# Optimization experiments

Hardware: AMD Instinct MI355X
Metric: run time of the kernel (lower is better)

## Reference

```python
import jax, jax.numpy as jnp
import numpy as np

N, E, D, R = 50000, 600000, 128, 16
SLOPE = 0.01  # torch default leaky_relu negative slope


def setup_inputs() -> dict:
    key = jax.random.key(0)
    ks = jax.random.split(key, 8)
    return {
        "nfeat": jax.random.normal(ks[0], (N, D), jnp.float32),
        "efeat": jax.random.normal(ks[1], (E, D), jnp.float32),
        # xavier_uniform-ish scale for relation weights / linear layers
        "relation_weight": jax.random.normal(ks[2], (R, D, D), jnp.float32) * (2.0 / np.sqrt(D)),
        "W_res": jax.random.normal(ks[3], (D, D), jnp.float32) / np.sqrt(D),
        "W_res2": jax.random.normal(ks[4], (D, D), jnp.float32) / np.sqrt(D),
        "src": jax.random.randint(ks[5], (E,), 0, N, dtype=jnp.int32),
        "dst": jax.random.randint(ks[6], (E,), 0, N, dtype=jnp.int32),
        "etype": jax.random.randint(ks[7], (E,), 0, R, dtype=jnp.int32),
    }


def reference(nfeat, efeat, relation_weight, W_res, W_res2, src, dst, etype):
    h = nfeat  # feat_drop = 0.0 -> identity
    e = efeat
    # bmm_maybe_select(h[src], W, etype) == (h @ W[r])[src] with r = etype.
    # Precompute all relation projections once: [R, N, D] (avoids E x D x D gather).
    proj = jnp.einsum('nd,rdf->rnf', h, relation_weight)
    t_r = proj[etype, src]   # [E, D]  (tail  * W_r)
    h_r = proj[etype, dst]   # [E, D]  (head  * W_r)
    att = jnp.sum(t_r * jnp.tanh(h_r + e), axis=-1)  # [E] per-edge attention logit
    # edge softmax over incoming edges of each destination node
    seg_max = jax.ops.segment_max(att, dst, num_segments=N)
    ex = jnp.exp(att - seg_max[dst])
    seg_sum = jax.ops.segment_sum(ex, dst, num_segments=N)
    a = ex / seg_sum[dst]                              # [E]
    # message passing: m = h[src] * a, aggregated by sum onto dst
    h_nb = jax.ops.segment_sum(h[src] * a[:, None], dst, num_segments=N)  # [N, D]
    out = (jax.nn.leaky_relu((h + h_nb) @ W_res.T, SLOPE)
           + jax.nn.leaky_relu((h * h_nb) @ W_res2.T, SLOPE))
    return out
```

## Files before the change

kernel.cpp:

```cpp
#include <hip/hip_runtime.h>

#define DF 128

__device__ __forceinline__ float lrelu(float x) { return x > 0.0f ? x : 0.01f * x; }

__global__ __launch_bounds__(256) void k_zero(int* __restrict__ deg,
                                              int* __restrict__ cur, int N) {
  int i = blockIdx.x * 256 + threadIdx.x;
  if (i < N) { deg[i] = 0; cur[i] = 0; }
}

__global__ __launch_bounds__(256) void k_hist(const int* __restrict__ dst,
                                              int* __restrict__ deg, int E) {
  int e = blockIdx.x * 256 + threadIdx.x;
  if (e < E) atomicAdd(&deg[dst[e]], 1);
}

__global__ __launch_bounds__(256) void k_scan1(const int* __restrict__ deg,
                                               int* __restrict__ excl,
                                               int* __restrict__ bsum, int N) {
  __shared__ int s[256];
  int tid = threadIdx.x;
  int i = blockIdx.x * 256 + tid;
  int v = (i < N) ? deg[i] : 0;
  s[tid] = v;
  __syncthreads();
  for (int d = 1; d < 256; d <<= 1) {
    int t = (tid >= d) ? s[tid - d] : 0;
    __syncthreads();
    s[tid] += t;
    __syncthreads();
  }
  int incl = s[tid];
  if (i < N) excl[i] = incl - v;
  if (tid == 255) bsum[blockIdx.x] = incl;
}

__global__ __launch_bounds__(256) void k_scan2(int* __restrict__ bsum, int nb) {
  __shared__ int s[256];
  __shared__ int carry;
  int tid = threadIdx.x;
  if (tid == 0) carry = 0;
  __syncthreads();
  for (int base = 0; base < nb; base += 256) {
    int i = base + tid;
    int v = (i < nb) ? bsum[i] : 0;
    s[tid] = v;
    __syncthreads();
    for (int d = 1; d < 256; d <<= 1) {
      int t = (tid >= d) ? s[tid - d] : 0;
      __syncthreads();
      s[tid] += t;
      __syncthreads();
    }
    int incl = s[tid];
    int c = carry;
    if (i < nb) bsum[i] = incl - v + c;
    __syncthreads();
    if (tid == 255) carry = c + s[255];
    __syncthreads();
  }
}

__global__ __launch_bounds__(256) void k_scan3(const int* __restrict__ excl,
                                               const int* __restrict__ bsum,
                                               int* __restrict__ off, int N, int E) {
  int i = blockIdx.x * 256 + threadIdx.x;
  if (i < N) off[i] = excl[i] + bsum[blockIdx.x];
  if (i == 0) off[N] = E;
}

__global__ __launch_bounds__(256) void k_fill(const int* __restrict__ dst,
                                              const int* __restrict__ off,
                                              int* __restrict__ cur,
                                              int* __restrict__ eid, int E) {
  int e = blockIdx.x * 256 + threadIdx.x;
  if (e >= E) return;
  int d = dst[e];
  int p = atomicAdd(&cur[d], 1);
  eid[off[d] + p] = e;
}

__global__ __launch_bounds__(256) void proj_gemm(const float* __restrict__ h,
                                                 const float* __restrict__ relW,
                                                 float* __restrict__ proj, int N,
                                                 int r0, long long out_rstride) {
  __shared__ float Bs[DF * DF];
  __shared__ float As[32 * DF];
  int r = r0 + blockIdx.y;
  const float* W = relW + (size_t)r * DF * DF;
  float* out = proj + (size_t)blockIdx.y * out_rstride;
  int n0 = blockIdx.x * 32;
  int t = threadIdx.x;

#pragma unroll
  for (int i = 0; i < 16; i++) {
    int idx = i * 256 + t;
    ((float4*)Bs)[idx] = ((const float4*)W)[idx];
  }
#pragma unroll
  for (int i = 0; i < 4; i++) {
    int idx = i * 256 + t;
    int row = idx >> 5, c4 = idx & 31;
    int n = n0 + row;
    float4 v = make_float4(0.f, 0.f, 0.f, 0.f);
    if (n < N) v = ((const float4*)(h + (size_t)n * DF))[c4];
    ((float4*)As)[idx] = v;
  }
  __syncthreads();

  int tc = t & 31, tr = t >> 5;
  float acc[4][4] = {};
#pragma unroll 4
  for (int k = 0; k < DF; k++) {
    float a0 = As[(tr * 4 + 0) * DF + k];
    float a1 = As[(tr * 4 + 1) * DF + k];
    float a2 = As[(tr * 4 + 2) * DF + k];
    float a3 = As[(tr * 4 + 3) * DF + k];
    float4 b = *(const float4*)&Bs[k * DF + tc * 4];
    acc[0][0] += a0 * b.x; acc[0][1] += a0 * b.y; acc[0][2] += a0 * b.z; acc[0][3] += a0 * b.w;
    acc[1][0] += a1 * b.x; acc[1][1] += a1 * b.y; acc[1][2] += a1 * b.z; acc[1][3] += a1 * b.w;
    acc[2][0] += a2 * b.x; acc[2][1] += a2 * b.y; acc[2][2] += a2 * b.z; acc[2][3] += a2 * b.w;
    acc[3][0] += a3 * b.x; acc[3][1] += a3 * b.y; acc[3][2] += a3 * b.z; acc[3][3] += a3 * b.w;
  }
#pragma unroll
  for (int i = 0; i < 4; i++) {
    int n = n0 + tr * 4 + i;
    if (n < N) {
      float4 o = make_float4(acc[i][0], acc[i][1], acc[i][2], acc[i][3]);
      *(float4*)&out[(size_t)n * DF + tc * 4] = o;
    }
  }
}

__global__ __launch_bounds__(256) void att_kernel(const float* __restrict__ proj,
                                                  const float* __restrict__ efeat,
                                                  const int* __restrict__ src,
                                                  const int* __restrict__ dst,
                                                  const int* __restrict__ etype,
                                                  float* __restrict__ att,
                                                  int E, long long rstride, int rsel) {
  int gid = blockIdx.x * 256 + threadIdx.x;
  int e = gid >> 6, lane = gid & 63;
  if (e >= E) return;
  int rt = etype[e];
  if (rsel >= 0 && rt != rsel) return;
  int s = src[e], d = dst[e];
  const float* pb = proj + (size_t)rt * (size_t)rstride;
  float2 tv = ((const float2*)(pb + (size_t)s * DF))[lane];
  float2 hv = ((const float2*)(pb + (size_t)d * DF))[lane];
  float2 ev = ((const float2*)(efeat + (size_t)e * DF))[lane];
  float p = tv.x * tanhf(hv.x + ev.x) + tv.y * tanhf(hv.y + ev.y);
  p += __shfl_down(p, 32);
  p += __shfl_down(p, 16);
  p += __shfl_down(p, 8);
  p += __shfl_down(p, 4);
  p += __shfl_down(p, 2);
  p += __shfl_down(p, 1);
  if (lane == 0) att[e] = p;
}

__global__ __launch_bounds__(256) void gather_kernel(const int* __restrict__ eid,
                                                     const int* __restrict__ off,
                                                     const int* __restrict__ src,
                                                     const float* __restrict__ att,
                                                     const float* __restrict__ nfeat,
                                                     float* __restrict__ h_nb, int N) {
  int node = blockIdx.x * 4 + (threadIdx.x >> 6);
  int lane = threadIdx.x & 63;
  if (node >= N) return;
  int s0 = off[node], s1 = off[node + 1];

  float m = -3.402823466e+38f;
  for (int j = s0 + lane; j < s1; j += 64) {
    float a = att[eid[j]];
    m = fmaxf(m, a);
  }
#pragma unroll
  for (int d = 32; d >= 1; d >>= 1) m = fmaxf(m, __shfl_xor(m, d));

  float2 acc = make_float2(0.f, 0.f);
  float ssum = 0.f;
  for (int j = s0; j < s1; j++) {
    int e = eid[j];
    float ex = expf(att[e] - m);
    int sv = src[e];
    float2 hv = ((const float2*)(nfeat + (size_t)sv * DF))[lane];
    acc.x += hv.x * ex;
    acc.y += hv.y * ex;
    ssum += ex;
  }
  float inv = (s1 > s0) ? 1.0f / ssum : 0.0f;
  float2 o = make_float2(acc.x * inv, acc.y * inv);
  ((float2*)(h_nb + (size_t)node * DF))[lane] = o;
}

__global__ __launch_bounds__(256) void out_gemm(const float* __restrict__ nfeat,
                                                const float* __restrict__ h_nb,
                                                const float* __restrict__ W,
                                                float* __restrict__ out, int N, int mode) {
  __shared__ float Ws[DF * 129];
  __shared__ float As[32 * DF];
  int n0 = blockIdx.x * 32;
  int t = threadIdx.x;
#pragma unroll
  for (int i = 0; i < 16; i++) {
    int idx = i * 256 + t;
    int j = idx >> 5, d4 = idx & 31;
    float4 v = ((const float4*)W)[idx];
    int b = j * 129 + d4 * 4;
    Ws[b + 0] = v.x; Ws[b + 1] = v.y; Ws[b + 2] = v.z; Ws[b + 3] = v.w;
  }
#pragma unroll
  for (int i = 0; i < 4; i++) {
    int idx = i * 256 + t;
    int row = idx >> 5, c4 = idx & 31;
    int n = n0 + row;
    float4 a = make_float4(0.f, 0.f, 0.f, 0.f);
    if (n < N) {
      float4 hv = ((const float4*)(nfeat + (size_t)n * DF))[c4];
      float4 bv = ((const float4*)(h_nb + (size_t)n * DF))[c4];
      if (mode == 0) a = make_float4(hv.x + bv.x, hv.y + bv.y, hv.z + bv.z, hv.w + bv.w);
      else           a = make_float4(hv.x * bv.x, hv.y * bv.y, hv.z * bv.z, hv.w * bv.w);
    }
    ((float4*)As)[idx] = a;
  }
  __syncthreads();

  int tc = t & 31, tr = t >> 5;
  float acc[4][4] = {};
#pragma unroll 4
  for (int k = 0; k < DF; k++) {
    float a0 = As[(tr * 4 + 0) * DF + k];
    float a1 = As[(tr * 4 + 1) * DF + k];
    float a2 = As[(tr * 4 + 2) * DF + k];
    float a3 = As[(tr * 4 + 3) * DF + k];
    float w0 = Ws[(tc * 4 + 0) * 129 + k];
    float w1 = Ws[(tc * 4 + 1) * 129 + k];
    float w2 = Ws[(tc * 4 + 2) * 129 + k];
    float w3 = Ws[(tc * 4 + 3) * 129 + k];
    acc[0][0] += a0 * w0; acc[0][1] += a0 * w1; acc[0][2] += a0 * w2; acc[0][3] += a0 * w3;
    acc[1][0] += a1 * w0; acc[1][1] += a1 * w1; acc[1][2] += a1 * w2; acc[1][3] += a1 * w3;
    acc[2][0] += a2 * w0; acc[2][1] += a2 * w1; acc[2][2] += a2 * w2; acc[2][3] += a2 * w3;
    acc[3][0] += a3 * w0; acc[3][1] += a3 * w1; acc[3][2] += a3 * w2; acc[3][3] += a3 * w3;
  }
#pragma unroll
  for (int i = 0; i < 4; i++) {
    int n = n0 + tr * 4 + i;
    if (n < N) {
      float4 o = make_float4(lrelu(acc[i][0]), lrelu(acc[i][1]),
                             lrelu(acc[i][2]), lrelu(acc[i][3]));
      float4* po = (float4*)&out[(size_t)n * DF + tc * 4];
      if (mode == 0) {
        *po = o;
      } else {
        float4 old = *po;
        *po = make_float4(old.x + o.x, old.y + o.y, old.z + o.z, old.w + o.w);
      }
    }
  }
}

extern "C" void kernel_launch(void* const* d_in, const int* in_sizes, int n_in,
                              void* d_out, int out_size, void* d_ws, size_t ws_size,
                              hipStream_t stream) {
  const float* nfeat  = (const float*)d_in[0];
  const float* efeat  = (const float*)d_in[1];
  const float* relW   = (const float*)d_in[2];
  const float* W_res  = (const float*)d_in[3];
  const float* W_res2 = (const float*)d_in[4];
  const int*   src    = (const int*)d_in[5];
  const int*   dst    = (const int*)d_in[6];
  const int*   etype  = (const int*)d_in[7];
  float* out = (float*)d_out;

  int N = in_sizes[0] / DF;
  int E = in_sizes[5];
  int R = in_sizes[2] / (DF * DF);

  int nblk256 = (N + 255) / 256;
  int eblk256 = (E + 255) / 256;

  char* w = (char*)d_ws;
  float* att  = (float*)w;  w += (size_t)E * 4;
  int*   eid  = (int*)w;    w += (size_t)E * 4;
  int*   deg  = (int*)w;    w += (size_t)N * 4;
  int*   excl = (int*)w;    w += (size_t)N * 4;
  int*   cur  = (int*)w;    w += (size_t)N * 4;
  int*   off  = (int*)w;    w += (size_t)(N + 1) * 4;
  int*   bsum = (int*)w;    w += (size_t)(nblk256 + 1) * 4;
  w = (char*)(((size_t)w + 255) & ~(size_t)255);
  float* h_nb = (float*)w;  w += (size_t)N * DF * 4;
  float* proj = (float*)w;
  size_t used = (size_t)(w - (char*)d_ws);
  size_t proj_full_bytes = (size_t)R * N * DF * 4;
  bool full = (ws_size >= used + proj_full_bytes);

  int row_tiles  = (N + 31) / 32;
  int att_blocks = (E + 3) / 4;
  int gat_blocks = (N + 3) / 4;

  k_zero<<<nblk256, 256, 0, stream>>>(deg, cur, N);
  k_hist<<<eblk256, 256, 0, stream>>>(dst, deg, E);
  k_scan1<<<nblk256, 256, 0, stream>>>(deg, excl, bsum, N);
  k_scan2<<<1, 256, 0, stream>>>(bsum, nblk256);
  k_scan3<<<nblk256, 256, 0, stream>>>(excl, bsum, off, N, E);
  k_fill<<<eblk256, 256, 0, stream>>>(dst, off, cur, eid, E);

  if (full) {
    proj_gemm<<<dim3(row_tiles, R), 256, 0, stream>>>(nfeat, relW, proj, N, 0,
                                                      (long long)N * DF);
    att_kernel<<<att_blocks, 256, 0, stream>>>(proj, efeat, src, dst, etype, att,
                                               E, (long long)N * DF, -1);
  } else {
    for (int r = 0; r < R; r++) {
      proj_gemm<<<dim3(row_tiles, 1), 256, 0, stream>>>(nfeat, relW, proj, N, r, 0);
      att_kernel<<<att_blocks, 256, 0, stream>>>(proj, efeat, src, dst, etype, att,
                                                 E, 0, r);
    }
  }

  gather_kernel<<<gat_blocks, 256, 0, stream>>>(eid, off, src, att, nfeat, h_nb, N);

  out_gemm<<<row_tiles, 256, 0, stream>>>(nfeat, h_nb, W_res,  out, N, 0);
  out_gemm<<<row_tiles, 256, 0, stream>>>(nfeat, h_nb, W_res2, out, N, 1);
}
```

Baseline: 1.284 ms.

## Use split-bf16 MFMA for relation projection GEMM instead of FP32 FMA

Replaces the scalar FP32 shared-memory GEMM for the per-relation projection with a matrix-core kernel. Inputs and relation weights are each split into high and low bf16 parts, and three bf16 MFMAs per tile approximate FP32 accuracy. New pre-pass kernels convert node features and pre-swizzle the weights into the MFMA operand layout. The aim is to cut the compute cost of the R×N×D×D projection, at the price of extra conversion passes, extra workspace and a small loss of precision.

```diff
diff --git a/kernel.cpp b/kernel.cpp
--- a/kernel.cpp
+++ b/kernel.cpp
@@ -2,7 +2,121 @@
 
 #define DF 128
 
+typedef __attribute__((ext_vector_type(8))) short short8;
+typedef __attribute__((ext_vector_type(4))) float floatx4;
+
 __device__ __forceinline__ float lrelu(float x) { return x > 0.0f ? x : 0.01f * x; }
+
+__device__ __forceinline__ unsigned short f2bf(float x) {
+  unsigned u = __float_as_uint(x);
+  unsigned r = (u >> 16) & 1u;
+  return (unsigned short)((u + 0x7fffu + r) >> 16);
+}
+__device__ __forceinline__ float bf2f(unsigned short h) {
+  return __uint_as_float(((unsigned)h) << 16);
+}
+
+__global__ __launch_bounds__(256) void k_convA(const float* __restrict__ x,
+                                               unsigned short* __restrict__ hi,
+                                               unsigned short* __restrict__ lo,
+                                               int total4) {
+  int i = blockIdx.x * 256 + threadIdx.x;
+  if (i >= total4) return;
+  float4 v = ((const float4*)x)[i];
+  ushort4 h, l;
+  h.x = f2bf(v.x); l.x = f2bf(v.x - bf2f(h.x));
+  h.y = f2bf(v.y); l.y = f2bf(v.y - bf2f(h.y));
+  h.z = f2bf(v.z); l.z = f2bf(v.z - bf2f(h.z));
+  h.w = f2bf(v.w); l.w = f2bf(v.w - bf2f(h.w));
+  ((ushort4*)hi)[i] = h;
+  ((ushort4*)lo)[i] = l;
+}
+
+__global__ __launch_bounds__(256) void k_convW(const float* __restrict__ W,
+                                               unsigned short* __restrict__ Wsw,
+                                               int R) {
+  int g = blockIdx.x * 256 + threadIdx.x;
+  int total = R * 8 * 4 * 64;
+  if (g >= total) return;
+  int lane = g & 63;
+  int kit  = (g >> 6) & 3;
+  int nt   = (g >> 8) & 7;
+  int r    = g >> 11;
+  int n = nt * 16 + (lane & 15);
+  int kbase = kit * 32 + (lane >> 4) * 8;
+  unsigned short hbuf[8], lbuf[8];
+#pragma unroll
+  for (int j = 0; j < 8; j++) {
+    float x = W[((size_t)r * DF + (kbase + j)) * DF + n];
+    unsigned short h = f2bf(x);
+    hbuf[j] = h;
+    lbuf[j] = f2bf(x - bf2f(h));
+  }
+  size_t base = (size_t)r * 32768 + (((nt * 4 + kit) * 64 + lane) * 8);
+  ((ushort4*)(Wsw + base))[0] = *(ushort4*)&hbuf[0];
+  ((ushort4*)(Wsw + base))[1] = *(ushort4*)&hbuf[4];
+  ((ushort4*)(Wsw + base + 16384))[0] = *(ushort4*)&lbuf[0];
+  ((ushort4*)(Wsw + base + 16384))[1] = *(ushort4*)&lbuf[4];
+}
+
+__global__ __launch_bounds__(256) void proj_mfma(const unsigned short* __restrict__ Ahi,
+                                                 const unsigned short* __restrict__ Alo,
+                                                 const unsigned short* __restrict__ Wsw,
+                                                 float* __restrict__ proj, int N,
+                                                 int r0, long long out_rstride) {
+  int t = threadIdx.x;
+  int wave = t >> 6, lane = t & 63;
+  int quad = lane >> 4, l15 = lane & 15;
+  int r = r0 + blockIdx.y;
+  float* out = proj + (size_t)blockIdx.y * out_rstride;
+  int mbase = blockIdx.x * 128 + wave * 32;
+
+  const unsigned short* wr = Wsw + (size_t)r * 32768;
+
+  floatx4 acc[2][8];
+#pragma unroll
+  for (int mt = 0; mt < 2; mt++)
+#pragma unroll
+    for (int nt = 0; nt < 8; nt++) acc[mt][nt] = (floatx4){0.f, 0.f, 0.f, 0.f};
+
+  int row0 = mbase + l15;       if (row0 >= N) row0 = N - 1;
+  int row1 = mbase + 16 + l15;  if (row1 >= N) row1 = N - 1;
+
+#pragma unroll
+  for (int kit = 0; kit < 4; kit++) {
+    int kcol = kit * 32 + quad * 8;
+    short8 ah0 = *(const short8*)(Ahi + (size_t)row0 * DF + kcol);
+    short8 al0 = *(const short8*)(Alo + (size_t)row0 * DF + kcol);
+    short8 ah1 = *(const short8*)(Ahi + (size_t)row1 * DF + kcol);
+    short8 al1 = *(const short8*)(Alo + (size_t)row1 * DF + kcol);
+#pragma unroll
+    for (int nt = 0; nt < 8; nt++) {
+      size_t boff = (size_t)(((nt * 4 + kit) * 64 + lane) * 8);
+      short8 bh = *(const short8*)(wr + boff);
+      short8 bl = *(const short8*)(wr + 16384 + boff);
+      acc[0][nt] = __builtin_amdgcn_mfma_f32_16x16x32_bf16(ah0, bh, acc[0][nt], 0, 0, 0);
+      acc[0][nt] = __builtin_amdgcn_mfma_f32_16x16x32_bf16(ah0, bl, acc[0][nt], 0, 0, 0);
+      acc[0][nt] = __builtin_amdgcn_mfma_f32_16x16x32_bf16(al0, bh, acc[0][nt], 0, 0, 0);
+      acc[1][nt] = __builtin_amdgcn_mfma_f32_16x16x32_bf16(ah1, bh, acc[1][nt], 0, 0, 0);
+      acc[1][nt] = __builtin_amdgcn_mfma_f32_16x16x32_bf16(ah1, bl, acc[1][nt], 0, 0, 0);
+      acc[1][nt] = __builtin_amdgcn_mfma_f32_16x16x32_bf16(al1, bh, acc[1][nt], 0, 0, 0);
+    }
+  }
+
+#pragma unroll
+  for (int mt = 0; mt < 2; mt++) {
+    int rbase = mbase + mt * 16 + quad * 4;
+#pragma unroll
+    for (int reg = 0; reg < 4; reg++) {
+      int row = rbase + reg;
+      if (row < N) {
+        float* orow = out + (size_t)row * DF + l15;
+#pragma unroll
+        for (int nt = 0; nt < 8; nt++) orow[nt * 16] = acc[mt][nt][reg];
+      }
+    }
+  }
+}
 
 __global__ __launch_bounds__(256) void k_zero(int* __restrict__ deg,
                                               int* __restrict__ cur, int N) {
@@ -79,58 +193,6 @@
   int d = dst[e];
   int p = atomicAdd(&cur[d], 1);
   eid[off[d] + p] = e;
-}
-
-__global__ __launch_bounds__(256) void proj_gemm(const float* __restrict__ h,
-                                                 const float* __restrict__ relW,
-                                                 float* __restrict__ proj, int N,
-                                                 int r0, long long out_rstride) {
-  __shared__ float Bs[DF * DF];
-  __shared__ float As[32 * DF];
-  int r = r0 + blockIdx.y;
-  const float* W = relW + (size_t)r * DF * DF;
-  float* out = proj + (size_t)blockIdx.y * out_rstride;
-  int n0 = blockIdx.x * 32;
-  int t = threadIdx.x;
-
-#pragma unroll
-  for (int i = 0; i < 16; i++) {
-    int idx = i * 256 + t;
-    ((float4*)Bs)[idx] = ((const float4*)W)[idx];
-  }
-#pragma unroll
-  for (int i = 0; i < 4; i++) {
-    int idx = i * 256 + t;
-    int row = idx >> 5, c4 = idx & 31;
-    int n = n0 + row;
-    float4 v = make_float4(0.f, 0.f, 0.f, 0.f);
-    if (n < N) v = ((const float4*)(h + (size_t)n * DF))[c4];
-    ((float4*)As)[idx] = v;
-  }
-  __syncthreads();
-
-  int tc = t & 31, tr = t >> 5;
-  float acc[4][4] = {};
-#pragma unroll 4
-  for (int k = 0; k < DF; k++) {
-    float a0 = As[(tr * 4 + 0) * DF + k];
-    float a1 = As[(tr * 4 + 1) * DF + k];
-    float a2 = As[(tr * 4 + 2) * DF + k];
-    float a3 = As[(tr * 4 + 3) * DF + k];
-    float4 b = *(const float4*)&Bs[k * DF + tc * 4];
-    acc[0][0] += a0 * b.x; acc[0][1] += a0 * b.y; acc[0][2] += a0 * b.z; acc[0][3] += a0 * b.w;
-    acc[1][0] += a1 * b.x; acc[1][1] += a1 * b.y; acc[1][2] += a1 * b.z; acc[1][3] += a1 * b.w;
-    acc[2][0] += a2 * b.x; acc[2][1] += a2 * b.y; acc[2][2] += a2 * b.z; acc[2][3] += a2 * b.w;
-    acc[3][0] += a3 * b.x; acc[3][1] += a3 * b.y; acc[3][2] += a3 * b.z; acc[3][3] += a3 * b.w;
-  }
-#pragma unroll
-  for (int i = 0; i < 4; i++) {
-    int n = n0 + tr * 4 + i;
-    if (n < N) {
-      float4 o = make_float4(acc[i][0], acc[i][1], acc[i][2], acc[i][3]);
-      *(float4*)&out[(size_t)n * DF + tc * 4] = o;
-    }
-  }
 }
 
 __global__ __launch_bounds__(256) void att_kernel(const float* __restrict__ proj,
@@ -290,6 +352,10 @@
   int*   off  = (int*)w;    w += (size_t)(N + 1) * 4;
   int*   bsum = (int*)w;    w += (size_t)(nblk256 + 1) * 4;
   w = (char*)(((size_t)w + 255) & ~(size_t)255);
+  unsigned short* Ahi = (unsigned short*)w; w += (size_t)N * DF * 2;
+  unsigned short* Alo = (unsigned short*)w; w += (size_t)N * DF * 2;
+  unsigned short* Wsw = (unsigned short*)w; w += (size_t)R * 32768 * 2;
+  w = (char*)(((size_t)w + 255) & ~(size_t)255);
   float* h_nb = (float*)w;  w += (size_t)N * DF * 4;
   float* proj = (float*)w;
   size_t used = (size_t)(w - (char*)d_ws);
@@ -297,8 +363,14 @@
   bool full = (ws_size >= used + proj_full_bytes);
 
   int row_tiles  = (N + 31) / 32;
+  int mfma_tiles = (N + 127) / 128;
   int att_blocks = (E + 3) / 4;
   int gat_blocks = (N + 3) / 4;
+
+  int a4 = N * DF / 4;
+  k_convA<<<(a4 + 255) / 256, 256, 0, stream>>>(nfeat, Ahi, Alo, a4);
+  int wgrp = R * 8 * 4 * 64;
+  k_convW<<<(wgrp + 255) / 256, 256, 0, stream>>>(relW, Wsw, R);
 
   k_zero<<<nblk256, 256, 0, stream>>>(deg, cur, N);
   k_hist<<<eblk256, 256, 0, stream>>>(dst, deg, E);
@@ -308,13 +380,13 @@
   k_fill<<<eblk256, 256, 0, stream>>>(dst, off, cur, eid, E);
 
   if (full) {
-    proj_gemm<<<dim3(row_tiles, R), 256, 0, stream>>>(nfeat, relW, proj, N, 0,
-                                                      (long long)N * DF);
+    proj_mfma<<<dim3(mfma_tiles, R), 256, 0, stream>>>(Ahi, Alo, Wsw, proj, N, 0,
+                                                       (long long)N * DF);
     att_kernel<<<att_blocks, 256, 0, stream>>>(proj, efeat, src, dst, etype, att,
                                                E, (long long)N * DF, -1);
   } else {
     for (int r = 0; r < R; r++) {
-      proj_gemm<<<dim3(row_tiles, 1), 256, 0, stream>>>(nfeat, relW, proj, N, r, 0);
+      proj_mfma<<<dim3(mfma_tiles, 1), 256, 0, stream>>>(Ahi, Alo, Wsw, proj, N, r, 0);
       att_kernel<<<att_blocks, 256, 0, stream>>>(proj, efeat, src, dst, etype, att,
                                                  E, 0, r);
     }
```

Result: faster. 1.099 ms (-14.4%).
